# Kernel optimization log

Measured on AMD Instinct MI355X. Metric: run time of the kernel, lower is better.

The kernel has to match this reference:

```python
import jax, jax.numpy as jnp
import numpy as np

D_MODEL = 768
NUM_HEADS = 12
D_K = D_MODEL // NUM_HEADS
D_FF = 3072
EPS = 1e-5


def _layer_norm(x, gamma, beta):
    mu = jnp.mean(x, axis=-1, keepdims=True)
    var = jnp.mean(jnp.square(x - mu), axis=-1, keepdims=True)
    return (x - mu) * jax.lax.rsqrt(var + EPS) * gamma + beta


def setup_inputs() -> dict:
    key = jax.random.key(0)
    ks = jax.random.split(key, 16)
    s = 1.0 / np.sqrt(D_MODEL)
    sf = 1.0 / np.sqrt(D_FF)
    inp = {
        "x": jax.random.normal(ks[0], (2, 2048, D_MODEL), dtype=jnp.float32),
        "Wq": jax.random.uniform(ks[1], (D_MODEL, D_MODEL), jnp.float32, -s, s),
        "bq": jax.random.uniform(ks[2], (D_MODEL,), jnp.float32, -s, s),
        "Wk": jax.random.uniform(ks[3], (D_MODEL, D_MODEL), jnp.float32, -s, s),
        "bk": jax.random.uniform(ks[4], (D_MODEL,), jnp.float32, -s, s),
        "Wv": jax.random.uniform(ks[5], (D_MODEL, D_MODEL), jnp.float32, -s, s),
        "bv": jax.random.uniform(ks[6], (D_MODEL,), jnp.float32, -s, s),
        "Wo": jax.random.uniform(ks[7], (D_MODEL, D_MODEL), jnp.float32, -s, s),
        "bo": jax.random.uniform(ks[8], (D_MODEL,), jnp.float32, -s, s),
        "W1": jax.random.uniform(ks[9], (D_MODEL, D_FF), jnp.float32, -s, s),
        "b1": jax.random.uniform(ks[10], (D_FF,), jnp.float32, -s, s),
        "W2": jax.random.uniform(ks[11], (D_FF, D_MODEL), jnp.float32, -sf, sf),
        "b2": jax.random.uniform(ks[12], (D_MODEL,), jnp.float32, -sf, sf),
        "g1": jnp.ones((D_MODEL,), jnp.float32),
        "be1": jnp.zeros((D_MODEL,), jnp.float32),
        "g2": jnp.ones((D_MODEL,), jnp.float32),
        "be2": jnp.zeros((D_MODEL,), jnp.float32),
    }
    return inp


def reference(x, Wq, bq, Wk, bk, Wv, bv, Wo, bo, W1, b1, W2, b2, g1, be1, g2, be2):
    B, S, _ = x.shape

    def split(h):  # (B,S,D) -> (B,H,S,Dk)
        return h.reshape(B, S, NUM_HEADS, D_K).transpose(0, 2, 1, 3)

    q = split(x @ Wq + bq)
    k = split(x @ Wk + bk)
    v = split(x @ Wv + bv)

    # naive attention: materialize full (B,H,S,S) scores as in the original
    scores = jnp.einsum("bhsd,bhtd->bhst", q, k) / np.sqrt(D_K)
    attn = jax.nn.softmax(scores, axis=-1)
    ctx = jnp.einsum("bhst,bhtd->bhsd", attn, v)
    ctx = ctx.transpose(0, 2, 1, 3).reshape(B, S, D_MODEL)
    attn_out = ctx @ Wo + bo

    x = _layer_norm(x + attn_out, g1, be1)
    ff = jax.nn.relu(x @ W1 + b1) @ W2 + b2
    x = _layer_norm(x + ff, g2, be2)
    return x
```

## Files before the change

### kernel.cpp

```cpp
#include <hip/hip_runtime.h>
#include <cstdint>


typedef unsigned short u16;
typedef unsigned int u32;
typedef __attribute__((ext_vector_type(4))) float f32x4;
typedef __attribute__((ext_vector_type(8))) short s16x8;
typedef __attribute__((ext_vector_type(4))) u16  u16x4;
typedef __attribute__((ext_vector_type(2))) u32  u32x2;

#define AS1 __attribute__((address_space(1)))
#define AS3 __attribute__((address_space(3)))

__device__ __forceinline__ u16 f2b(float f) {
  union { float f; unsigned u; } v; v.f = f;
  unsigned r = v.u + 0x7FFFu + ((v.u >> 16) & 1u);
  return (u16)(r >> 16);
}

__device__ __forceinline__ void gl_lds16(const void* g, void* lds_uniform_base) {
  __builtin_amdgcn_global_load_lds((const AS1 void*)g, (AS3 void*)lds_uniform_base, 16, 0, 0);
}

__device__ __forceinline__ f32x4 mfma16(s16x8 a, s16x8 b, f32x4 c) {
  return __builtin_amdgcn_mfma_f32_16x16x32_bf16(a, b, c, 0, 0, 0);
}

__device__ __forceinline__ u32 cvt_pk_bf16(float lo, float hi) {
  u32 r;
  asm("v_cvt_pk_bf16_f32 %0, %1, %2" : "=v"(r) : "v"(lo), "v"(hi));
  return r;
}


__global__ __launch_bounds__(256) void transpose_conv(const float* __restrict__ W,
                                                      u16* __restrict__ Wt, int K, int N) {
  __shared__ float tile[32][33];
  int n0 = blockIdx.x * 32, k0 = blockIdx.y * 32;
  int x = threadIdx.x, y = threadIdx.y;
#pragma unroll
  for (int yy = 0; yy < 32; yy += 8)
    tile[y + yy][x] = W[(size_t)(k0 + y + yy) * N + n0 + x];
  __syncthreads();
#pragma unroll
  for (int yy = 0; yy < 32; yy += 8)
    Wt[(size_t)(n0 + y + yy) * K + k0 + x] = f2b(tile[x][y + yy]);
}

__global__ __launch_bounds__(256) void transpose_v(const u16* __restrict__ Vh,
                                                   u16* __restrict__ Vt) {
  __shared__ u16 tile[32][33];
  int bh = blockIdx.z;
  int d0 = blockIdx.x * 32, s0 = blockIdx.y * 32;
  const u16* src = Vh + (size_t)bh * 2048 * 64;
  u16* dst = Vt + (size_t)bh * 64 * 2048;
  int x = threadIdx.x, y = threadIdx.y;
#pragma unroll
  for (int yy = 0; yy < 32; yy += 8)
    tile[y + yy][x] = src[(size_t)(s0 + y + yy) * 64 + d0 + x];
  __syncthreads();
#pragma unroll
  for (int yy = 0; yy < 32; yy += 8)
    dst[(size_t)(d0 + y + yy) * 2048 + s0 + x] = tile[x][y + yy];
}

__global__ __launch_bounds__(256) void conv_bf16(const float* __restrict__ in,
                                                 u16* __restrict__ out) {
  size_t i = ((size_t)blockIdx.x * 256 + threadIdx.x) * 4;
  f32x4 v = *(const f32x4*)(in + i);
  u16x4 o;
#pragma unroll
  for (int k = 0; k < 4; ++k) o[k] = f2b(v[k]);
  *(u16x4*)(out + i) = o;
}

__global__ void concat_bias(const float* __restrict__ bq, const float* __restrict__ bk,
                            const float* __restrict__ bv, float* __restrict__ o) {
  int i = blockIdx.x * 256 + threadIdx.x;
  o[i] = (i < 768) ? bq[i] : (i < 1536) ? bk[i - 768] : bv[i - 1536];
}

template <int MODE>
__global__ __launch_bounds__(256) void gemm_bt(const u16* __restrict__ A,
                                               const u16* __restrict__ Bt,
                                               const float* __restrict__ bias,
                                               float* __restrict__ Cf, u16* __restrict__ Cb,
                                               u16* __restrict__ Qo, u16* __restrict__ Ko,
                                               u16* __restrict__ Vo, int M, int N, int K,
                                               int Klen) {
  __shared__ __align__(16) u16 lsA[128 * 64];
  __shared__ __align__(16) u16 lsB[128 * 64];
  const int tid = threadIdx.x;
  const int lane = tid & 63, wave = tid >> 6;
  const int lr = lane & 15, lh = lane >> 4;
  const int wr = wave >> 1, wc = wave & 1;
  const int m0 = blockIdx.y * 128;
  const int n0 = blockIdx.x * 128;
  const int kB = blockIdx.z * Klen;

  f32x4 acc[4][4];
#pragma unroll
  for (int i = 0; i < 4; ++i)
#pragma unroll
    for (int j = 0; j < 4; ++j) acc[i][j] = f32x4{0.f, 0.f, 0.f, 0.f};

  const size_t aBase = (size_t)m0 * K;
  const size_t bBase = (size_t)n0 * K;
  const int srow8 = tid >> 3;
  const int scolb = ((tid & 7) * 16) ^ ((srow8 & 7) << 4);
  const int xk = (lr & 7) << 4;

  for (int kt = kB; kt < kB + Klen; kt += 64) {
#pragma unroll
    for (int i = 0; i < 4; ++i) {
      int row = i * 32 + srow8;
      int ldsOff = i * 4096 + wave * 1024;
      gl_lds16(A + aBase + (size_t)row * K + kt + (scolb >> 1), (char*)lsA + ldsOff);
      gl_lds16(Bt + bBase + (size_t)row * K + kt + (scolb >> 1), (char*)lsB + ldsOff);
    }
    __syncthreads();
    const char* baA = (const char*)lsA;
    const char* baB = (const char*)lsB;
#pragma unroll
    for (int ks = 0; ks < 2; ++ks) {
      int cb = (ks * 64 + lh * 16) ^ xk;
      s16x8 a[4], b[4];
#pragma unroll
      for (int i = 0; i < 4; ++i) {
        a[i] = *(const s16x8*)(baA + (wr * 64 + i * 16 + lr) * 128 + cb);
        b[i] = *(const s16x8*)(baB + (wc * 64 + i * 16 + lr) * 128 + cb);
      }
#pragma unroll
      for (int i = 0; i < 4; ++i)
#pragma unroll
        for (int j = 0; j < 4; ++j) acc[i][j] = mfma16(a[i], b[j], acc[i][j]);
    }
    __syncthreads();
  }

  float* CfP = Cf + (size_t)blockIdx.z * M * N;
#pragma unroll
  for (int i = 0; i < 4; ++i) {
    int growb = m0 + wr * 64 + i * 16 + lh * 4;
#pragma unroll
    for (int j = 0; j < 4; ++j) {
      int col = n0 + wc * 64 + j * 16 + lr;
      float bv = (MODE != 0 || blockIdx.z == 0) ? bias[col] : 0.f;
#pragma unroll
      for (int q = 0; q < 4; ++q) {
        int grow = growb + q;
        float v = acc[i][j][q] + bv;
        if (MODE == 0) {
          CfP[(size_t)grow * N + col] = v;
        } else if (MODE == 1) {
          Cb[(size_t)grow * N + col] = f2b(fmaxf(v, 0.f));
        } else {
          int sel = col / 768;
          int c2 = col - sel * 768;
          int h = c2 >> 6, d = c2 & 63;
          int b = grow >> 11, s = grow & 2047;
          size_t idx = (((size_t)(b * 12 + h)) * 2048 + s) * 64 + d;
          float vv = (sel == 0) ? v * 0.1803368801f : v;
          u16* dst = (sel == 0) ? Qo : (sel == 1) ? Ko : Vo;
          dst[idx] = f2b(vv);
        }
      }
    }
  }
}

__global__ __launch_bounds__(512) void attn(const u16* __restrict__ Qh,
                                            const u16* __restrict__ Kh,
                                            const u16* __restrict__ Vt,
                                            float* __restrict__ Op,
                                            float* __restrict__ ml,
                                            int nbh, int ntile) {
  __shared__ __align__(16) u16 lsK[2][64 * 64];
  __shared__ __align__(16) u16 lsV[2][64 * 64];
  __shared__ __align__(16) u16 lsP[8][16 * 64];
  const int tid = threadIdx.x, lane = tid & 63, wave = tid >> 6;
  const int lr = lane & 15, lh = lane >> 4;

  int bx = blockIdx.x, bh = blockIdx.y, z = blockIdx.z;
  {
    int total = 16 * nbh * 2;
    if ((total & 7) == 0) {
      int lin = bx + 16 * (bh + nbh * z);
      int nl = (lin & 7) * (total >> 3) + (lin >> 3);
      bx = nl & 15;
      bh = (nl >> 4) % nbh;
      z = nl / (16 * nbh);
    }
  }
  const int q0 = bx * 128 + wave * 16;
  const size_t kvBase = (size_t)bh * 2048 * 64;
  const int tB = z * ntile;

  const int srow = tid >> 3;
  const int scol = (((tid & 7) * 16) ^ ((srow & 7) << 4)) >> 1;
  const u16* kSrcBase = Kh + kvBase + (size_t)srow * 64 + scol;
  const u16* vSrcBase = Vt + kvBase + (size_t)srow * 2048 + scol;

  s16x8 qf[2];
#pragma unroll
  for (int ks = 0; ks < 2; ++ks)
    qf[ks] = *(const s16x8*)(Qh + kvBase + (size_t)(q0 + lr) * 64 + ks * 32 + lh * 8);

  f32x4 oacc[4];
  float mrow = -1e30f, lsum = 0.f;
#pragma unroll
  for (int d = 0; d < 4; ++d) oacc[d] = f32x4{0.f, 0.f, 0.f, 0.f};

  gl_lds16(kSrcBase + (size_t)tB * 4096, (char*)lsK[0] + wave * 1024);
  gl_lds16(vSrcBase + tB * 64,           (char*)lsV[0] + wave * 1024);

  for (int it = 0; it < ntile; ++it) {
    const int cur = it & 1;
    __syncthreads();

    s16x8 kb[2][4];
#pragma unroll
    for (int ks = 0; ks < 2; ++ks)
#pragma unroll
      for (int j = 0; j < 4; ++j) {
        int r = j * 16 + lr;
        kb[ks][j] = *(const s16x8*)((const char*)lsK[cur] + r * 128 +
                                    ((ks * 64 + lh * 16) ^ ((r & 7) << 4)));
      }

    if (it + 1 < ntile) {
      int t = tB + it + 1;
      gl_lds16(kSrcBase + (size_t)t * 4096, (char*)lsK[cur ^ 1] + wave * 1024);
      gl_lds16(vSrcBase + t * 64,           (char*)lsV[cur ^ 1] + wave * 1024);
    }

    f32x4 st[4];
#pragma unroll
    for (int j = 0; j < 4; ++j) st[j] = f32x4{0.f, 0.f, 0.f, 0.f};
    __builtin_amdgcn_s_setprio(1);
#pragma unroll
    for (int ks = 0; ks < 2; ++ks)
#pragma unroll
      for (int j = 0; j < 4; ++j) st[j] = mfma16(kb[ks][j], qf[ks], st[j]);
    __builtin_amdgcn_s_setprio(0);

    float mx;
    {
      float a0 = fmaxf(fmaxf(st[0][0], st[0][1]), fmaxf(st[0][2], st[0][3]));
      float a1 = fmaxf(fmaxf(st[1][0], st[1][1]), fmaxf(st[1][2], st[1][3]));
      float a2 = fmaxf(fmaxf(st[2][0], st[2][1]), fmaxf(st[2][2], st[2][3]));
      float a3 = fmaxf(fmaxf(st[3][0], st[3][1]), fmaxf(st[3][2], st[3][3]));
      mx = fmaxf(fmaxf(a0, a1), fmaxf(a2, a3));
      mx = fmaxf(mx, __shfl_xor(mx, 16));
      mx = fmaxf(mx, __shfl_xor(mx, 32));
    }
    if (__any(mx > mrow + 11.f)) {
      float mn = fmaxf(mrow, mx);
      float al = exp2f(mrow - mn);
      mrow = mn;
      lsum *= al;
#pragma unroll
      for (int d = 0; d < 4; ++d)
#pragma unroll
        for (int q = 0; q < 4; ++q) oacc[d][q] *= al;
    }

    float ps = 0.f;
#pragma unroll
    for (int j = 0; j < 4; ++j) {
      float p0 = exp2f(st[j][0] - mrow);
      float p1 = exp2f(st[j][1] - mrow);
      float p2 = exp2f(st[j][2] - mrow);
      float p3 = exp2f(st[j][3] - mrow);
      ps += (p0 + p1) + (p2 + p3);
      u32x2 pk;
      pk.x = cvt_pk_bf16(p0, p1);
      pk.y = cvt_pk_bf16(p2, p3);
      *(u32x2*)((char*)lsP[wave] + lr * 128 + ((j * 32 + lh * 8) ^ ((lr & 7) << 4))) = pk;
    }
    ps += __shfl_xor(ps, 16);
    ps += __shfl_xor(ps, 32);
    lsum += ps;

    __builtin_amdgcn_s_setprio(1);
#pragma unroll
    for (int ks = 0; ks < 2; ++ks) {
      s16x8 pa = *(const s16x8*)((const char*)lsP[wave] + lr * 128 +
                                 ((ks * 64 + lh * 16) ^ ((lr & 7) << 4)));
#pragma unroll
      for (int d = 0; d < 4; ++d) {
        int r = d * 16 + lr;
        s16x8 vb = *(const s16x8*)((const char*)lsV[cur] + r * 128 +
                                   ((ks * 64 + lh * 16) ^ ((r & 7) << 4)));
        oacc[d] = mfma16(vb, pa, oacc[d]);
      }
    }
    __builtin_amdgcn_s_setprio(0);
  }

  {
    int s = q0 + lr;
    size_t r = ((size_t)z * nbh + bh) * 2048 + s;
#pragma unroll
    for (int d = 0; d < 4; ++d)
      *(f32x4*)(Op + r * 64 + d * 16 + lh * 4) = oacc[d];
    if (lh == 0) { ml[r * 2] = mrow; ml[r * 2 + 1] = lsum; }
  }
}

__global__ __launch_bounds__(256) void attn_combine(const float* __restrict__ Op,
                                                    const float* __restrict__ ml,
                                                    u16* __restrict__ ctx, int nbh) {
  size_t i = (size_t)blockIdx.x * 256 + threadIdx.x;
  int d4 = (int)(i & 15);
  size_t rs = i >> 4;
  size_t zs = (size_t)nbh * 2048;
  float m0 = ml[rs * 2],        l0 = ml[rs * 2 + 1];
  float m1 = ml[(zs + rs) * 2], l1 = ml[(zs + rs) * 2 + 1];
  float mx = fmaxf(m0, m1);
  float a0 = exp2f(m0 - mx), a1 = exp2f(m1 - mx);
  float inv = 1.f / (l0 * a0 + l1 * a1);
  a0 *= inv; a1 *= inv;
  f32x4 o0 = *(const f32x4*)(Op + rs * 64 + d4 * 4);
  f32x4 o1 = *(const f32x4*)(Op + (zs + rs) * 64 + d4 * 4);
  int bh = (int)(rs >> 11), s = (int)(rs & 2047);
  int b = bh / 12, h = bh - b * 12;
  u16x4 r;
#pragma unroll
  for (int k = 0; k < 4; ++k) r[k] = f2b(o0[k] * a0 + o1[k] * a1);
  *(u16x4*)(ctx + ((size_t)(b * 2048 + s)) * 768 + h * 64 + d4 * 4) = r;
}

template <int NP>
__global__ __launch_bounds__(256) void resid_ln(const float* __restrict__ xin,
                                                const float* __restrict__ yp,
                                                size_t pstride,
                                                const float* __restrict__ gamma,
                                                const float* __restrict__ beta,
                                                float* __restrict__ outf,
                                                u16* __restrict__ outb) {
  const int row = blockIdx.x, t = threadIdx.x;
  const size_t base = (size_t)row * 768;
  float v[3], s = 0.f, s2 = 0.f;
#pragma unroll
  for (int k = 0; k < 3; ++k) {
    int c = t + k * 256;
    float val = xin[base + c];
#pragma unroll
    for (int p = 0; p < NP; ++p) val += yp[p * pstride + base + c];
    v[k] = val; s += val; s2 += val * val;
  }
#pragma unroll
  for (int off = 32; off > 0; off >>= 1) {
    s += __shfl_down(s, off, 64);
    s2 += __shfl_down(s2, off, 64);
  }
  __shared__ float red[8];
  int lane = t & 63, wave = t >> 6;
  if (lane == 0) { red[wave] = s; red[4 + wave] = s2; }
  __syncthreads();
  s = red[0] + red[1] + red[2] + red[3];
  s2 = red[4] + red[5] + red[6] + red[7];
  const float inv = 1.f / 768.f;
  float mu = s * inv;
  float var = fmaxf(s2 * inv - mu * mu, 0.f);
  float rs = rsqrtf(var + 1e-5f);
#pragma unroll
  for (int k = 0; k < 3; ++k) {
    int c = t + k * 256;
    float o = (v[k] - mu) * rs * gamma[c] + beta[c];
    if (outf) outf[base + c] = o;
    if (outb) outb[base + c] = f2b(o);
  }
}

extern "C" void kernel_launch(void* const* d_in, const int* in_sizes, int n_in,
                              void* d_out, int out_size, void* d_ws, size_t ws_size,
                              hipStream_t stream) {
  const float* x   = (const float*)d_in[0];
  const float* Wq  = (const float*)d_in[1];
  const float* bq  = (const float*)d_in[2];
  const float* Wk  = (const float*)d_in[3];
  const float* bk  = (const float*)d_in[4];
  const float* Wv  = (const float*)d_in[5];
  const float* bv  = (const float*)d_in[6];
  const float* Wo  = (const float*)d_in[7];
  const float* bo  = (const float*)d_in[8];
  const float* W1  = (const float*)d_in[9];
  const float* b1  = (const float*)d_in[10];
  const float* W2  = (const float*)d_in[11];
  const float* b2  = (const float*)d_in[12];
  const float* g1  = (const float*)d_in[13];
  const float* be1 = (const float*)d_in[14];
  const float* g2  = (const float*)d_in[15];
  const float* be2 = (const float*)d_in[16];
  float* out = (float*)d_out;

  const int M = in_sizes[0] / 768;
  const int B = M / 2048;
  const int nbh = B * 12;

  char* ws = (char*)d_ws;
  size_t off = 0;
  auto alloc = [&](size_t bytes) -> void* {
    void* p = ws + off;
    off += (bytes + 255) & ~(size_t)255;
    return p;
  };
  u16*   Wqkv_t = (u16*)alloc((size_t)2304 * 768 * 2);
  u16*   Wo_t   = (u16*)alloc((size_t)768 * 768 * 2);
  u16*   W1_t   = (u16*)alloc((size_t)3072 * 768 * 2);
  u16*   W2_t   = (u16*)alloc((size_t)768 * 3072 * 2);
  float* bqkv   = (float*)alloc(2304 * 4);
  u16*   Xb     = (u16*)alloc((size_t)M * 768 * 2);
  u16*   Qh     = (u16*)alloc((size_t)M * 768 * 2);
  u16*   Kh     = (u16*)alloc((size_t)M * 768 * 2);
  u16*   Vh     = (u16*)alloc((size_t)M * 768 * 2);
  u16*   Vt     = (u16*)alloc((size_t)M * 768 * 2);

  size_t opElems = (size_t)2 * nbh * 2048 * 64;
  size_t mlElems = (size_t)2 * nbh * 2048 * 2;
  size_t attnBytes = (opElems + mlElems) * 4;
  size_t pstride = (size_t)M * 768;
  size_t fixedRest = pstride * 4  + pstride * 2  +
                     (size_t)M * 3072 * 2  + 4096 ;
  size_t need4 = off + ((pstride * 4 * 4 > attnBytes ? pstride * 4 * 4 : attnBytes)) + fixedRest;
  const int SPLIT2 = (ws_size >= need4) ? 4 : 2;
  size_t regionBytes = pstride * 4 * SPLIT2;
  if (regionBytes < attnBytes) regionBytes = attnBytes;
  float* region = (float*)alloc(regionBytes);
  float* Op   = region;
  float* ml   = region + opElems;
  float* ffnPart  = region;
  float* projPart = (float*)Qh;
  float* x1f  = (float*)alloc(pstride * 4);
  u16*   x1b  = (u16*)alloc(pstride * 2);
  u16*   hb   = (u16*)alloc((size_t)M * 3072 * 2);
  u16*   ctx  = Xb;

  dim3 tb(32, 8);
  transpose_conv<<<dim3(24, 24), tb, 0, stream>>>(Wq, Wqkv_t, 768, 768);
  transpose_conv<<<dim3(24, 24), tb, 0, stream>>>(Wk, Wqkv_t + (size_t)768 * 768, 768, 768);
  transpose_conv<<<dim3(24, 24), tb, 0, stream>>>(Wv, Wqkv_t + (size_t)1536 * 768, 768, 768);
  transpose_conv<<<dim3(24, 24), tb, 0, stream>>>(Wo, Wo_t, 768, 768);
  transpose_conv<<<dim3(96, 24), tb, 0, stream>>>(W1, W1_t, 768, 3072);
  transpose_conv<<<dim3(24, 96), tb, 0, stream>>>(W2, W2_t, 3072, 768);
  concat_bias<<<9, 256, 0, stream>>>(bq, bk, bv, bqkv);
  conv_bf16<<<(M * 768) / 1024, 256, 0, stream>>>(x, Xb);

  gemm_bt<2><<<dim3(2304 / 128, M / 128), 256, 0, stream>>>(
      Xb, Wqkv_t, bqkv, nullptr, nullptr, Qh, Kh, Vh, M, 2304, 768, 768);

  transpose_v<<<dim3(2, 64, nbh), tb, 0, stream>>>(Vh, Vt);

  attn<<<dim3(16, nbh, 2), 512, 0, stream>>>(Qh, Kh, Vt, Op, ml, nbh, 16);
  attn_combine<<<nbh * 128, 256, 0, stream>>>(Op, ml, ctx, nbh);

  gemm_bt<0><<<dim3(768 / 128, M / 128, 2), 256, 0, stream>>>(
      ctx, Wo_t, bo, projPart, nullptr, nullptr, nullptr, nullptr, M, 768, 768, 384);

  resid_ln<2><<<M, 256, 0, stream>>>(x, projPart, pstride, g1, be1, x1f, x1b);

  gemm_bt<1><<<dim3(3072 / 128, M / 128), 256, 0, stream>>>(
      x1b, W1_t, b1, nullptr, hb, nullptr, nullptr, nullptr, M, 3072, 768, 768);

  if (SPLIT2 == 4) {
    gemm_bt<0><<<dim3(768 / 128, M / 128, 4), 256, 0, stream>>>(
        hb, W2_t, b2, ffnPart, nullptr, nullptr, nullptr, nullptr, M, 768, 3072, 768);
    resid_ln<4><<<M, 256, 0, stream>>>(x1f, ffnPart, pstride, g2, be2, out, nullptr);
  } else {
    gemm_bt<0><<<dim3(768 / 128, M / 128, 2), 256, 0, stream>>>(
        hb, W2_t, b2, ffnPart, nullptr, nullptr, nullptr, nullptr, M, 768, 3072, 1536);
    resid_ln<2><<<M, 256, 0, stream>>>(x1f, ffnPart, pstride, g2, be2, out, nullptr);
  }
}
```

Baseline: 231.8 us.

## Fuse prep kernels, double-buffer GEMM LDS, and give attention waves two query tiles

Eight weight-transpose, bias-concat and input-conversion launches become one prep kernel, cutting launch overhead. The GEMM now double-buffers its LDS tiles, so the next K tile loads while the current one is multiplied, and one barrier per iteration is dropped. The attention kernel moves to 256 threads, with each wave handling 32 query rows instead of 16, so every K/V fragment read from LDS is reused across two MFMA tiles. The trade-off is more registers and twice the GEMM LDS footprint, which may lower occupancy.

```diff
diff --git a/kernel.cpp b/kernel.cpp
--- a/kernel.cpp
+++ b/kernel.cpp
@@ -32,19 +32,51 @@
   return r;
 }
 
-
-__global__ __launch_bounds__(256) void transpose_conv(const float* __restrict__ W,
-                                                      u16* __restrict__ Wt, int K, int N) {
-  __shared__ float tile[32][33];
-  int n0 = blockIdx.x * 32, k0 = blockIdx.y * 32;
-  int x = threadIdx.x, y = threadIdx.y;
-#pragma unroll
-  for (int yy = 0; yy < 32; yy += 8)
-    tile[y + yy][x] = W[(size_t)(k0 + y + yy) * N + n0 + x];
-  __syncthreads();
-#pragma unroll
-  for (int yy = 0; yy < 32; yy += 8)
-    Wt[(size_t)(n0 + y + yy) * K + k0 + x] = f2b(tile[x][y + yy]);
+__global__ __launch_bounds__(256) void prep(
+    const float* __restrict__ Wq, const float* __restrict__ Wk,
+    const float* __restrict__ Wv, const float* __restrict__ Wo,
+    const float* __restrict__ W1, const float* __restrict__ W2,
+    const float* __restrict__ bq, const float* __restrict__ bk,
+    const float* __restrict__ bv, const float* __restrict__ x,
+    u16* __restrict__ Wqkv_t, u16* __restrict__ Wo_t,
+    u16* __restrict__ W1_t, u16* __restrict__ W2_t,
+    float* __restrict__ bqkv, u16* __restrict__ Xb, int convBlocks) {
+  __shared__ float ts[32][33];
+  const int bid = blockIdx.x;
+  const int tx = threadIdx.x, ty = threadIdx.y;
+  if (bid < 6912) {
+    const float* W; u16* Wt; int K, N, tile;
+    if (bid < 2304) {
+      int w = bid / 576; tile = bid - w * 576; K = 768; N = 768;
+      W = (w == 0) ? Wq : (w == 1) ? Wk : (w == 2) ? Wv : Wo;
+      Wt = (w < 3) ? Wqkv_t + (size_t)w * 768 * 768 : Wo_t;
+    } else if (bid < 4608) {
+      tile = bid - 2304; K = 768; N = 3072; W = W1; Wt = W1_t;
+    } else {
+      tile = bid - 4608; K = 3072; N = 768; W = W2; Wt = W2_t;
+    }
+    int ntx = N >> 5;
+    int n0 = (tile % ntx) * 32, k0 = (tile / ntx) * 32;
+#pragma unroll
+    for (int yy = 0; yy < 32; yy += 8)
+      ts[ty + yy][tx] = W[(size_t)(k0 + ty + yy) * N + n0 + tx];
+    __syncthreads();
+#pragma unroll
+    for (int yy = 0; yy < 32; yy += 8)
+      Wt[(size_t)(n0 + ty + yy) * K + k0 + tx] = f2b(ts[tx][ty + yy]);
+  } else if (bid < 6912 + convBlocks) {
+    int t = ty * 32 + tx;
+    size_t i = ((size_t)(bid - 6912) * 256 + t) * 4;
+    f32x4 v = *(const f32x4*)(x + i);
+    u16x4 o;
+#pragma unroll
+    for (int k = 0; k < 4; ++k) o[k] = f2b(v[k]);
+    *(u16x4*)(Xb + i) = o;
+  } else {
+    int t = ty * 32 + tx;
+    int i = (bid - 6912 - convBlocks) * 256 + t;
+    if (i < 2304) bqkv[i] = (i < 768) ? bq[i] : (i < 1536) ? bk[i - 768] : bv[i - 1536];
+  }
 }
 
 __global__ __launch_bounds__(256) void transpose_v(const u16* __restrict__ Vh,
@@ -64,22 +96,6 @@
     dst[(size_t)(d0 + y + yy) * 2048 + s0 + x] = tile[x][y + yy];
 }
 
-__global__ __launch_bounds__(256) void conv_bf16(const float* __restrict__ in,
-                                                 u16* __restrict__ out) {
-  size_t i = ((size_t)blockIdx.x * 256 + threadIdx.x) * 4;
-  f32x4 v = *(const f32x4*)(in + i);
-  u16x4 o;
-#pragma unroll
-  for (int k = 0; k < 4; ++k) o[k] = f2b(v[k]);
-  *(u16x4*)(out + i) = o;
-}
-
-__global__ void concat_bias(const float* __restrict__ bq, const float* __restrict__ bk,
-                            const float* __restrict__ bv, float* __restrict__ o) {
-  int i = blockIdx.x * 256 + threadIdx.x;
-  o[i] = (i < 768) ? bq[i] : (i < 1536) ? bk[i - 768] : bv[i - 1536];
-}
-
 template <int MODE>
 __global__ __launch_bounds__(256) void gemm_bt(const u16* __restrict__ A,
                                                const u16* __restrict__ Bt,
@@ -88,8 +104,8 @@
                                                u16* __restrict__ Qo, u16* __restrict__ Ko,
                                                u16* __restrict__ Vo, int M, int N, int K,
                                                int Klen) {
-  __shared__ __align__(16) u16 lsA[128 * 64];
-  __shared__ __align__(16) u16 lsB[128 * 64];
+  __shared__ __align__(16) u16 lsA[2][128 * 64];
+  __shared__ __align__(16) u16 lsB[2][128 * 64];
   const int tid = threadIdx.x;
   const int lane = tid & 63, wave = tid >> 6;
   const int lr = lane & 15, lh = lane >> 4;
@@ -107,20 +123,27 @@
   const size_t aBase = (size_t)m0 * K;
   const size_t bBase = (size_t)n0 * K;
   const int srow8 = tid >> 3;
-  const int scolb = ((tid & 7) * 16) ^ ((srow8 & 7) << 4);
+  const int scolE = (((tid & 7) * 16) ^ ((srow8 & 7) << 4)) >> 1;
   const int xk = (lr & 7) << 4;
 
-  for (int kt = kB; kt < kB + Klen; kt += 64) {
+  auto stage = [&](int buf, int kt) {
 #pragma unroll
     for (int i = 0; i < 4; ++i) {
       int row = i * 32 + srow8;
-      int ldsOff = i * 4096 + wave * 1024;
-      gl_lds16(A + aBase + (size_t)row * K + kt + (scolb >> 1), (char*)lsA + ldsOff);
-      gl_lds16(Bt + bBase + (size_t)row * K + kt + (scolb >> 1), (char*)lsB + ldsOff);
-    }
+      int ldsOff = buf * 16384 + i * 4096 + wave * 1024;
+      gl_lds16(A + aBase + (size_t)row * K + kt + scolE, (char*)lsA + ldsOff);
+      gl_lds16(Bt + bBase + (size_t)row * K + kt + scolE, (char*)lsB + ldsOff);
+    }
+  };
+
+  const int nk = Klen >> 6;
+  stage(0, kB);
+  for (int t = 0; t < nk; ++t) {
+    const int cur = t & 1;
     __syncthreads();
-    const char* baA = (const char*)lsA;
-    const char* baB = (const char*)lsB;
+    if (t + 1 < nk) stage(cur ^ 1, kB + (t + 1) * 64);
+    const char* baA = (const char*)lsA + cur * 16384;
+    const char* baB = (const char*)lsB + cur * 16384;
 #pragma unroll
     for (int ks = 0; ks < 2; ++ks) {
       int cb = (ks * 64 + lh * 16) ^ xk;
@@ -135,7 +158,6 @@
 #pragma unroll
         for (int j = 0; j < 4; ++j) acc[i][j] = mfma16(a[i], b[j], acc[i][j]);
     }
-    __syncthreads();
   }
 
   float* CfP = Cf + (size_t)blockIdx.z * M * N;
@@ -169,15 +191,15 @@
   }
 }
 
-__global__ __launch_bounds__(512) void attn(const u16* __restrict__ Qh,
-                                            const u16* __restrict__ Kh,
-                                            const u16* __restrict__ Vt,
-                                            float* __restrict__ Op,
-                                            float* __restrict__ ml,
-                                            int nbh, int ntile) {
+__global__ __launch_bounds__(256, 3) void attn(const u16* __restrict__ Qh,
+                                               const u16* __restrict__ Kh,
+                                               const u16* __restrict__ Vt,
+                                               float* __restrict__ Op,
+                                               float* __restrict__ ml,
+                                               int nbh, int ntile) {
   __shared__ __align__(16) u16 lsK[2][64 * 64];
   __shared__ __align__(16) u16 lsV[2][64 * 64];
-  __shared__ __align__(16) u16 lsP[8][16 * 64];
+  __shared__ __align__(16) u16 lsP[4][32 * 64];
   const int tid = threadIdx.x, lane = tid & 63, wave = tid >> 6;
   const int lr = lane & 15, lh = lane >> 4;
 
@@ -192,28 +214,42 @@
       z = nl / (16 * nbh);
     }
   }
-  const int q0 = bx * 128 + wave * 16;
+  const int q0 = bx * 128 + wave * 32;
   const size_t kvBase = (size_t)bh * 2048 * 64;
   const int tB = z * ntile;
 
   const int srow = tid >> 3;
-  const int scol = (((tid & 7) * 16) ^ ((srow & 7) << 4)) >> 1;
-  const u16* kSrcBase = Kh + kvBase + (size_t)srow * 64 + scol;
-  const u16* vSrcBase = Vt + kvBase + (size_t)srow * 2048 + scol;
-
-  s16x8 qf[2];
-#pragma unroll
-  for (int ks = 0; ks < 2; ++ks)
-    qf[ks] = *(const s16x8*)(Qh + kvBase + (size_t)(q0 + lr) * 64 + ks * 32 + lh * 8);
-
-  f32x4 oacc[4];
-  float mrow = -1e30f, lsum = 0.f;
-#pragma unroll
-  for (int d = 0; d < 4; ++d) oacc[d] = f32x4{0.f, 0.f, 0.f, 0.f};
-
-  gl_lds16(kSrcBase + (size_t)tB * 4096, (char*)lsK[0] + wave * 1024);
-  gl_lds16(vSrcBase + tB * 64,           (char*)lsV[0] + wave * 1024);
-
+  const int scolE = (((tid & 7) * 16) ^ ((srow & 7) << 4)) >> 1;
+  const u16* kSrc = Kh + kvBase + (size_t)srow * 64 + scolE;
+  const u16* vSrc = Vt + kvBase + (size_t)srow * 2048 + scolE;
+
+  s16x8 qf[2][2];
+#pragma unroll
+  for (int i = 0; i < 2; ++i)
+#pragma unroll
+    for (int ks = 0; ks < 2; ++ks)
+      qf[i][ks] = *(const s16x8*)(Qh + kvBase + (size_t)(q0 + i * 16 + lr) * 64 +
+                                  ks * 32 + lh * 8);
+
+  f32x4 oacc[2][4];
+  float mrow[2], lsum[2];
+#pragma unroll
+  for (int i = 0; i < 2; ++i) {
+    mrow[i] = -1e30f; lsum[i] = 0.f;
+#pragma unroll
+    for (int d = 0; d < 4; ++d) oacc[i][d] = f32x4{0.f, 0.f, 0.f, 0.f};
+  }
+
+  auto stageKV = [&](int buf, int t) {
+#pragma unroll
+    for (int ii = 0; ii < 2; ++ii) {
+      int ldsOff = ii * 4096 + wave * 1024;
+      gl_lds16(kSrc + (size_t)(t * 64 + ii * 32) * 64, (char*)lsK[buf] + ldsOff);
+      gl_lds16(vSrc + (size_t)ii * 32 * 2048 + t * 64, (char*)lsV[buf] + ldsOff);
+    }
+  };
+
+  stageKV(0, tB);
   for (int it = 0; it < ntile; ++it) {
     const int cur = it & 1;
     __syncthreads();
@@ -228,83 +264,98 @@
                                     ((ks * 64 + lh * 16) ^ ((r & 7) << 4)));
       }
 
-    if (it + 1 < ntile) {
-      int t = tB + it + 1;
-      gl_lds16(kSrcBase + (size_t)t * 4096, (char*)lsK[cur ^ 1] + wave * 1024);
-      gl_lds16(vSrcBase + t * 64,           (char*)lsV[cur ^ 1] + wave * 1024);
-    }
-
-    f32x4 st[4];
-#pragma unroll
-    for (int j = 0; j < 4; ++j) st[j] = f32x4{0.f, 0.f, 0.f, 0.f};
+    if (it + 1 < ntile) stageKV(cur ^ 1, tB + it + 1);
+
+    f32x4 st[2][4];
+#pragma unroll
+    for (int i = 0; i < 2; ++i)
+#pragma unroll
+      for (int j = 0; j < 4; ++j) st[i][j] = f32x4{0.f, 0.f, 0.f, 0.f};
     __builtin_amdgcn_s_setprio(1);
 #pragma unroll
     for (int ks = 0; ks < 2; ++ks)
 #pragma unroll
-      for (int j = 0; j < 4; ++j) st[j] = mfma16(kb[ks][j], qf[ks], st[j]);
+      for (int j = 0; j < 4; ++j)
+#pragma unroll
+        for (int i = 0; i < 2; ++i)
+          st[i][j] = mfma16(kb[ks][j], qf[i][ks], st[i][j]);
     __builtin_amdgcn_s_setprio(0);
 
-    float mx;
-    {
-      float a0 = fmaxf(fmaxf(st[0][0], st[0][1]), fmaxf(st[0][2], st[0][3]));
-      float a1 = fmaxf(fmaxf(st[1][0], st[1][1]), fmaxf(st[1][2], st[1][3]));
-      float a2 = fmaxf(fmaxf(st[2][0], st[2][1]), fmaxf(st[2][2], st[2][3]));
-      float a3 = fmaxf(fmaxf(st[3][0], st[3][1]), fmaxf(st[3][2], st[3][3]));
-      mx = fmaxf(fmaxf(a0, a1), fmaxf(a2, a3));
-      mx = fmaxf(mx, __shfl_xor(mx, 16));
-      mx = fmaxf(mx, __shfl_xor(mx, 32));
-    }
-    if (__any(mx > mrow + 11.f)) {
-      float mn = fmaxf(mrow, mx);
-      float al = exp2f(mrow - mn);
-      mrow = mn;
-      lsum *= al;
-#pragma unroll
-      for (int d = 0; d < 4; ++d)
-#pragma unroll
-        for (int q = 0; q < 4; ++q) oacc[d][q] *= al;
-    }
-
-    float ps = 0.f;
-#pragma unroll
-    for (int j = 0; j < 4; ++j) {
-      float p0 = exp2f(st[j][0] - mrow);
-      float p1 = exp2f(st[j][1] - mrow);
-      float p2 = exp2f(st[j][2] - mrow);
-      float p3 = exp2f(st[j][3] - mrow);
-      ps += (p0 + p1) + (p2 + p3);
-      u32x2 pk;
-      pk.x = cvt_pk_bf16(p0, p1);
-      pk.y = cvt_pk_bf16(p2, p3);
-      *(u32x2*)((char*)lsP[wave] + lr * 128 + ((j * 32 + lh * 8) ^ ((lr & 7) << 4))) = pk;
-    }
-    ps += __shfl_xor(ps, 16);
-    ps += __shfl_xor(ps, 32);
-    lsum += ps;
+    float mx[2];
+    bool need = false;
+#pragma unroll
+    for (int i = 0; i < 2; ++i) {
+      float a0 = fmaxf(fmaxf(st[i][0][0], st[i][0][1]), fmaxf(st[i][0][2], st[i][0][3]));
+      float a1 = fmaxf(fmaxf(st[i][1][0], st[i][1][1]), fmaxf(st[i][1][2], st[i][1][3]));
+      float a2 = fmaxf(fmaxf(st[i][2][0], st[i][2][1]), fmaxf(st[i][2][2], st[i][2][3]));
+      float a3 = fmaxf(fmaxf(st[i][3][0], st[i][3][1]), fmaxf(st[i][3][2], st[i][3][3]));
+      float m = fmaxf(fmaxf(a0, a1), fmaxf(a2, a3));
+      m = fmaxf(m, __shfl_xor(m, 16));
+      m = fmaxf(m, __shfl_xor(m, 32));
+      mx[i] = m;
+      need = need || (m > mrow[i] + 11.f);
+    }
+    if (__any(need)) {
+#pragma unroll
+      for (int i = 0; i < 2; ++i) {
+        float mn = fmaxf(mrow[i], mx[i]);
+        float al = exp2f(mrow[i] - mn);
+        mrow[i] = mn;
+        lsum[i] *= al;
+#pragma unroll
+        for (int d = 0; d < 4; ++d)
+#pragma unroll
+          for (int q = 0; q < 4; ++q) oacc[i][d][q] *= al;
+      }
+    }
+#pragma unroll
+    for (int i = 0; i < 2; ++i) {
+      float ps = 0.f;
+#pragma unroll
+      for (int j = 0; j < 4; ++j) {
+        float p0 = exp2f(st[i][j][0] - mrow[i]);
+        float p1 = exp2f(st[i][j][1] - mrow[i]);
+        float p2 = exp2f(st[i][j][2] - mrow[i]);
+        float p3 = exp2f(st[i][j][3] - mrow[i]);
+        ps += (p0 + p1) + (p2 + p3);
+        u32x2 pk;
+        pk.x = cvt_pk_bf16(p0, p1);
+        pk.y = cvt_pk_bf16(p2, p3);
+        *(u32x2*)((char*)lsP[wave] + (i * 16 + lr) * 128 +
+                  ((j * 32 + lh * 8) ^ ((lr & 7) << 4))) = pk;
+      }
+      ps += __shfl_xor(ps, 16);
+      ps += __shfl_xor(ps, 32);
+      lsum[i] += ps;
+    }
 
     __builtin_amdgcn_s_setprio(1);
 #pragma unroll
     for (int ks = 0; ks < 2; ++ks) {
-      s16x8 pa = *(const s16x8*)((const char*)lsP[wave] + lr * 128 +
-                                 ((ks * 64 + lh * 16) ^ ((lr & 7) << 4)));
+      s16x8 pa0 = *(const s16x8*)((const char*)lsP[wave] + lr * 128 +
+                                  ((ks * 64 + lh * 16) ^ ((lr & 7) << 4)));
+      s16x8 pa1 = *(const s16x8*)((const char*)lsP[wave] + (16 + lr) * 128 +
+                                  ((ks * 64 + lh * 16) ^ ((lr & 7) << 4)));
 #pragma unroll
       for (int d = 0; d < 4; ++d) {
         int r = d * 16 + lr;
         s16x8 vb = *(const s16x8*)((const char*)lsV[cur] + r * 128 +
                                    ((ks * 64 + lh * 16) ^ ((r & 7) << 4)));
-        oacc[d] = mfma16(vb, pa, oacc[d]);
+        oacc[0][d] = mfma16(vb, pa0, oacc[0][d]);
+        oacc[1][d] = mfma16(vb, pa1, oacc[1][d]);
       }
     }
     __builtin_amdgcn_s_setprio(0);
   }
 
-  {
-    int s = q0 + lr;
+#pragma unroll
+  for (int i = 0; i < 2; ++i) {
+    int s = q0 + i * 16 + lr;
     size_t r = ((size_t)z * nbh + bh) * 2048 + s;
 #pragma unroll
     for (int d = 0; d < 4; ++d)
-      *(f32x4*)(Op + r * 64 + d * 16 + lh * 4) = oacc[d];
-    if (lh == 0) { ml[r * 2] = mrow; ml[r * 2 + 1] = lsum; }
+      *(f32x4*)(Op + r * 64 + d * 16 + lh * 4) = oacc[i][d];
+    if (lh == 0) { ml[r * 2] = mrow[i]; ml[r * 2 + 1] = lsum[i]; }
   }
 }
 
@@ -423,7 +474,7 @@
   size_t attnBytes = (opElems + mlElems) * 4;
   size_t pstride = (size_t)M * 768;
   size_t fixedRest = pstride * 4  + pstride * 2  +
-                     (size_t)M * 3072 * 2  + 4096 ;
+                     (size_t)M * 3072 * 2  + 4096;
   size_t need4 = off + ((pstride * 4 * 4 > attnBytes ? pstride * 4 * 4 : attnBytes)) + fixedRest;
   const int SPLIT2 = (ws_size >= need4) ? 4 : 2;
   size_t regionBytes = pstride * 4 * SPLIT2;
@@ -439,21 +490,17 @@
   u16*   ctx  = Xb;
 
   dim3 tb(32, 8);
-  transpose_conv<<<dim3(24, 24), tb, 0, stream>>>(Wq, Wqkv_t, 768, 768);
-  transpose_conv<<<dim3(24, 24), tb, 0, stream>>>(Wk, Wqkv_t + (size_t)768 * 768, 768, 768);
-  transpose_conv<<<dim3(24, 24), tb, 0, stream>>>(Wv, Wqkv_t + (size_t)1536 * 768, 768, 768);
-  transpose_conv<<<dim3(24, 24), tb, 0, stream>>>(Wo, Wo_t, 768, 768);
-  transpose_conv<<<dim3(96, 24), tb, 0, stream>>>(W1, W1_t, 768, 3072);
-  transpose_conv<<<dim3(24, 96), tb, 0, stream>>>(W2, W2_t, 3072, 768);
-  concat_bias<<<9, 256, 0, stream>>>(bq, bk, bv, bqkv);
-  conv_bf16<<<(M * 768) / 1024, 256, 0, stream>>>(x, Xb);
+  const int convBlocks = (M * 768) / 1024;
+  prep<<<6912 + convBlocks + 9, tb, 0, stream>>>(
+      Wq, Wk, Wv, Wo, W1, W2, bq, bk, bv, x,
+      Wqkv_t, Wo_t, W1_t, W2_t, bqkv, Xb, convBlocks);
 
   gemm_bt<2><<<dim3(2304 / 128, M / 128), 256, 0, stream>>>(
       Xb, Wqkv_t, bqkv, nullptr, nullptr, Qh, Kh, Vh, M, 2304, 768, 768);
 
   transpose_v<<<dim3(2, 64, nbh), tb, 0, stream>>>(Vh, Vt);
 
-  attn<<<dim3(16, nbh, 2), 512, 0, stream>>>(Qh, Kh, Vt, Op, ml, nbh, 16);
+  attn<<<dim3(16, nbh, 2), 256, 0, stream>>>(Qh, Kh, Vt, Op, ml, nbh, 16);
   attn_combine<<<nbh * 128, 256, 0, stream>>>(Op, ml, ctx, nbh);
 
   gemm_bt<0><<<dim3(768 / 128, M / 128, 2), 256, 0, stream>>>(
```

New measurement: 218.8 us. -5.6%, faster.

## Merge prep kernels, swizzle GEMM block order, and allow 4-way attention KV split

Applied to the files above, without the earlier changes.

Folds the six weight transpose-convert launches, the bias concat and the input bf16 conversion into one prep kernel that dispatches on block index, cutting launch count. Adds an XCD-aware block remap to all GEMM launches so neighbouring tiles land on the same die for L2 reuse. Lets attention split the key range four ways when workspace allows, with a templated combine kernel merging the partials. The deeper split adds partial-output traffic and combine work in exchange for more parallel blocks.

```diff
diff --git a/kernel.cpp b/kernel.cpp
--- a/kernel.cpp
+++ b/kernel.cpp
@@ -32,19 +32,51 @@
   return r;
 }
 
-
-__global__ __launch_bounds__(256) void transpose_conv(const float* __restrict__ W,
-                                                      u16* __restrict__ Wt, int K, int N) {
-  __shared__ float tile[32][33];
-  int n0 = blockIdx.x * 32, k0 = blockIdx.y * 32;
-  int x = threadIdx.x, y = threadIdx.y;
-#pragma unroll
-  for (int yy = 0; yy < 32; yy += 8)
-    tile[y + yy][x] = W[(size_t)(k0 + y + yy) * N + n0 + x];
-  __syncthreads();
-#pragma unroll
-  for (int yy = 0; yy < 32; yy += 8)
-    Wt[(size_t)(n0 + y + yy) * K + k0 + x] = f2b(tile[x][y + yy]);
+__global__ __launch_bounds__(256) void prep(
+    const float* __restrict__ Wq, const float* __restrict__ Wk,
+    const float* __restrict__ Wv, const float* __restrict__ Wo,
+    const float* __restrict__ W1, const float* __restrict__ W2,
+    const float* __restrict__ bq, const float* __restrict__ bk,
+    const float* __restrict__ bv, const float* __restrict__ x,
+    u16* __restrict__ Wqkv_t, u16* __restrict__ Wo_t,
+    u16* __restrict__ W1_t, u16* __restrict__ W2_t,
+    float* __restrict__ bqkv, u16* __restrict__ Xb, int convBlocks) {
+  __shared__ float ts[32][33];
+  const int bid = blockIdx.x;
+  const int tx = threadIdx.x, ty = threadIdx.y;
+  if (bid < 6912) {
+    const float* W; u16* Wt; int K, N, tile;
+    if (bid < 2304) {
+      int w = bid / 576; tile = bid - w * 576; K = 768; N = 768;
+      W = (w == 0) ? Wq : (w == 1) ? Wk : (w == 2) ? Wv : Wo;
+      Wt = (w < 3) ? Wqkv_t + (size_t)w * 768 * 768 : Wo_t;
+    } else if (bid < 4608) {
+      tile = bid - 2304; K = 768; N = 3072; W = W1; Wt = W1_t;
+    } else {
+      tile = bid - 4608; K = 3072; N = 768; W = W2; Wt = W2_t;
+    }
+    int ntx = N >> 5;
+    int n0 = (tile % ntx) * 32, k0 = (tile / ntx) * 32;
+#pragma unroll
+    for (int yy = 0; yy < 32; yy += 8)
+      ts[ty + yy][tx] = W[(size_t)(k0 + ty + yy) * N + n0 + tx];
+    __syncthreads();
+#pragma unroll
+    for (int yy = 0; yy < 32; yy += 8)
+      Wt[(size_t)(n0 + ty + yy) * K + k0 + tx] = f2b(ts[tx][ty + yy]);
+  } else if (bid < 6912 + convBlocks) {
+    int t = ty * 32 + tx;
+    size_t i = ((size_t)(bid - 6912) * 256 + t) * 4;
+    f32x4 v = *(const f32x4*)(x + i);
+    u16x4 o;
+#pragma unroll
+    for (int k = 0; k < 4; ++k) o[k] = f2b(v[k]);
+    *(u16x4*)(Xb + i) = o;
+  } else {
+    int t = ty * 32 + tx;
+    int i = (bid - 6912 - convBlocks) * 256 + t;
+    if (i < 2304) bqkv[i] = (i < 768) ? bq[i] : (i < 1536) ? bk[i - 768] : bv[i - 1536];
+  }
 }
 
 __global__ __launch_bounds__(256) void transpose_v(const u16* __restrict__ Vh,
@@ -62,22 +94,6 @@
 #pragma unroll
   for (int yy = 0; yy < 32; yy += 8)
     dst[(size_t)(d0 + y + yy) * 2048 + s0 + x] = tile[x][y + yy];
-}
-
-__global__ __launch_bounds__(256) void conv_bf16(const float* __restrict__ in,
-                                                 u16* __restrict__ out) {
-  size_t i = ((size_t)blockIdx.x * 256 + threadIdx.x) * 4;
-  f32x4 v = *(const f32x4*)(in + i);
-  u16x4 o;
-#pragma unroll
-  for (int k = 0; k < 4; ++k) o[k] = f2b(v[k]);
-  *(u16x4*)(out + i) = o;
-}
-
-__global__ void concat_bias(const float* __restrict__ bq, const float* __restrict__ bk,
-                            const float* __restrict__ bv, float* __restrict__ o) {
-  int i = blockIdx.x * 256 + threadIdx.x;
-  o[i] = (i < 768) ? bq[i] : (i < 1536) ? bk[i - 768] : bv[i - 1536];
 }
 
 template <int MODE>
@@ -94,9 +110,25 @@
   const int lane = tid & 63, wave = tid >> 6;
   const int lr = lane & 15, lh = lane >> 4;
   const int wr = wave >> 1, wc = wave & 1;
-  const int m0 = blockIdx.y * 128;
-  const int n0 = blockIdx.x * 128;
-  const int kB = blockIdx.z * Klen;
+
+  int bx, by, bz;
+  {
+    int nx = gridDim.x, ny = gridDim.y, nz = gridDim.z;
+    int total = nx * ny * nz;
+    int lin = blockIdx.x + nx * (blockIdx.y + ny * blockIdx.z);
+    if ((total & 7) == 0) {
+      int key = (lin & 7) * (total >> 3) + (lin >> 3);
+      by = key % ny;
+      int t2 = key / ny;
+      bz = t2 % nz;
+      bx = t2 / nz;
+    } else {
+      bx = blockIdx.x; by = blockIdx.y; bz = blockIdx.z;
+    }
+  }
+  const int m0 = by * 128;
+  const int n0 = bx * 128;
+  const int kB = bz * Klen;
 
   f32x4 acc[4][4];
 #pragma unroll
@@ -107,7 +139,7 @@
   const size_t aBase = (size_t)m0 * K;
   const size_t bBase = (size_t)n0 * K;
   const int srow8 = tid >> 3;
-  const int scolb = ((tid & 7) * 16) ^ ((srow8 & 7) << 4);
+  const int scolE = (((tid & 7) * 16) ^ ((srow8 & 7) << 4)) >> 1;
   const int xk = (lr & 7) << 4;
 
   for (int kt = kB; kt < kB + Klen; kt += 64) {
@@ -115,8 +147,8 @@
     for (int i = 0; i < 4; ++i) {
       int row = i * 32 + srow8;
       int ldsOff = i * 4096 + wave * 1024;
-      gl_lds16(A + aBase + (size_t)row * K + kt + (scolb >> 1), (char*)lsA + ldsOff);
-      gl_lds16(Bt + bBase + (size_t)row * K + kt + (scolb >> 1), (char*)lsB + ldsOff);
+      gl_lds16(A + aBase + (size_t)row * K + kt + scolE, (char*)lsA + ldsOff);
+      gl_lds16(Bt + bBase + (size_t)row * K + kt + scolE, (char*)lsB + ldsOff);
     }
     __syncthreads();
     const char* baA = (const char*)lsA;
@@ -138,14 +170,14 @@
     __syncthreads();
   }
 
-  float* CfP = Cf + (size_t)blockIdx.z * M * N;
+  float* CfP = Cf + (size_t)bz * M * N;
 #pragma unroll
   for (int i = 0; i < 4; ++i) {
     int growb = m0 + wr * 64 + i * 16 + lh * 4;
 #pragma unroll
     for (int j = 0; j < 4; ++j) {
       int col = n0 + wc * 64 + j * 16 + lr;
-      float bv = (MODE != 0 || blockIdx.z == 0) ? bias[col] : 0.f;
+      float bv = (MODE != 0 || bz == 0) ? bias[col] : 0.f;
 #pragma unroll
       for (int q = 0; q < 4; ++q) {
         int grow = growb + q;
@@ -183,7 +215,8 @@
 
   int bx = blockIdx.x, bh = blockIdx.y, z = blockIdx.z;
   {
-    int total = 16 * nbh * 2;
+    int nz = gridDim.z;
+    int total = 16 * nbh * nz;
     if ((total & 7) == 0) {
       int lin = bx + 16 * (bh + nbh * z);
       int nl = (lin & 7) * (total >> 3) + (lin >> 3);
@@ -308,6 +341,7 @@
   }
 }
 
+template <int NZ>
 __global__ __launch_bounds__(256) void attn_combine(const float* __restrict__ Op,
                                                     const float* __restrict__ ml,
                                                     u16* __restrict__ ctx, int nbh) {
@@ -315,19 +349,30 @@
   int d4 = (int)(i & 15);
   size_t rs = i >> 4;
   size_t zs = (size_t)nbh * 2048;
-  float m0 = ml[rs * 2],        l0 = ml[rs * 2 + 1];
-  float m1 = ml[(zs + rs) * 2], l1 = ml[(zs + rs) * 2 + 1];
-  float mx = fmaxf(m0, m1);
-  float a0 = exp2f(m0 - mx), a1 = exp2f(m1 - mx);
-  float inv = 1.f / (l0 * a0 + l1 * a1);
-  a0 *= inv; a1 *= inv;
-  f32x4 o0 = *(const f32x4*)(Op + rs * 64 + d4 * 4);
-  f32x4 o1 = *(const f32x4*)(Op + (zs + rs) * 64 + d4 * 4);
+  float m[NZ], l[NZ];
+  float mx = -1e30f;
+#pragma unroll
+  for (int p = 0; p < NZ; ++p) {
+    m[p] = ml[(p * zs + rs) * 2];
+    l[p] = ml[(p * zs + rs) * 2 + 1];
+    mx = fmaxf(mx, m[p]);
+  }
+  float wsum = 0.f, a[NZ];
+#pragma unroll
+  for (int p = 0; p < NZ; ++p) { a[p] = exp2f(m[p] - mx); wsum += l[p] * a[p]; }
+  float inv = 1.f / wsum;
+  f32x4 o = f32x4{0.f, 0.f, 0.f, 0.f};
+#pragma unroll
+  for (int p = 0; p < NZ; ++p) {
+    f32x4 op = *(const f32x4*)(Op + (p * zs + rs) * 64 + d4 * 4);
+#pragma unroll
+    for (int k = 0; k < 4; ++k) o[k] += op[k] * a[p];
+  }
   int bh = (int)(rs >> 11), s = (int)(rs & 2047);
   int b = bh / 12, h = bh - b * 12;
   u16x4 r;
 #pragma unroll
-  for (int k = 0; k < 4; ++k) r[k] = f2b(o0[k] * a0 + o1[k] * a1);
+  for (int k = 0; k < 4; ++k) r[k] = f2b(o[k] * inv);
   *(u16x4*)(ctx + ((size_t)(b * 2048 + s)) * 768 + h * 64 + d4 * 4) = r;
 }
 
@@ -418,19 +463,24 @@
   u16*   Vh     = (u16*)alloc((size_t)M * 768 * 2);
   u16*   Vt     = (u16*)alloc((size_t)M * 768 * 2);
 
-  size_t opElems = (size_t)2 * nbh * 2048 * 64;
-  size_t mlElems = (size_t)2 * nbh * 2048 * 2;
-  size_t attnBytes = (opElems + mlElems) * 4;
   size_t pstride = (size_t)M * 768;
   size_t fixedRest = pstride * 4  + pstride * 2  +
-                     (size_t)M * 3072 * 2  + 4096 ;
-  size_t need4 = off + ((pstride * 4 * 4 > attnBytes ? pstride * 4 * 4 : attnBytes)) + fixedRest;
-  const int SPLIT2 = (ws_size >= need4) ? 4 : 2;
-  size_t regionBytes = pstride * 4 * SPLIT2;
-  if (regionBytes < attnBytes) regionBytes = attnBytes;
+                     (size_t)M * 3072 * 2  + 4096;
+  auto attnBytes = [&](int nz) {
+    return (size_t)nz * nbh * 2048 * (64 + 2) * 4;
+  };
+  size_t reg4 = attnBytes(4) > pstride * 16 ? attnBytes(4) : pstride * 16;
+  int ZSPLIT, FSPLIT;
+  size_t regionBytes;
+  if (off + reg4 + fixedRest <= ws_size) {
+    ZSPLIT = 4; FSPLIT = 4; regionBytes = reg4;
+  } else {
+    ZSPLIT = 2; FSPLIT = 2;
+    regionBytes = attnBytes(2) > pstride * 8 ? attnBytes(2) : pstride * 8;
+  }
   float* region = (float*)alloc(regionBytes);
   float* Op   = region;
-  float* ml   = region + opElems;
+  float* ml   = region + (size_t)ZSPLIT * nbh * 2048 * 64;
   float* ffnPart  = region;
   float* projPart = (float*)Qh;
   float* x1f  = (float*)alloc(pstride * 4);
@@ -439,22 +489,21 @@
   u16*   ctx  = Xb;
 
   dim3 tb(32, 8);
-  transpose_conv<<<dim3(24, 24), tb, 0, stream>>>(Wq, Wqkv_t, 768, 768);
-  transpose_conv<<<dim3(24, 24), tb, 0, stream>>>(Wk, Wqkv_t + (size_t)768 * 768, 768, 768);
-  transpose_conv<<<dim3(24, 24), tb, 0, stream>>>(Wv, Wqkv_t + (size_t)1536 * 768, 768, 768);
-  transpose_conv<<<dim3(24, 24), tb, 0, stream>>>(Wo, Wo_t, 768, 768);
-  transpose_conv<<<dim3(96, 24), tb, 0, stream>>>(W1, W1_t, 768, 3072);
-  transpose_conv<<<dim3(24, 96), tb, 0, stream>>>(W2, W2_t, 3072, 768);
-  concat_bias<<<9, 256, 0, stream>>>(bq, bk, bv, bqkv);
-  conv_bf16<<<(M * 768) / 1024, 256, 0, stream>>>(x, Xb);
+  const int convBlocks = (M * 768) / 1024;
+  prep<<<6912 + convBlocks + 9, tb, 0, stream>>>(
+      Wq, Wk, Wv, Wo, W1, W2, bq, bk, bv, x,
+      Wqkv_t, Wo_t, W1_t, W2_t, bqkv, Xb, convBlocks);
 
   gemm_bt<2><<<dim3(2304 / 128, M / 128), 256, 0, stream>>>(
       Xb, Wqkv_t, bqkv, nullptr, nullptr, Qh, Kh, Vh, M, 2304, 768, 768);
 
   transpose_v<<<dim3(2, 64, nbh), tb, 0, stream>>>(Vh, Vt);
 
-  attn<<<dim3(16, nbh, 2), 512, 0, stream>>>(Qh, Kh, Vt, Op, ml, nbh, 16);
-  attn_combine<<<nbh * 128, 256, 0, stream>>>(Op, ml, ctx, nbh);
+  attn<<<dim3(16, nbh, ZSPLIT), 512, 0, stream>>>(Qh, Kh, Vt, Op, ml, nbh, 32 / ZSPLIT);
+  if (ZSPLIT == 4)
+    attn_combine<4><<<nbh * 128, 256, 0, stream>>>(Op, ml, ctx, nbh);
+  else
+    attn_combine<2><<<nbh * 128, 256, 0, stream>>>(Op, ml, ctx, nbh);
 
   gemm_bt<0><<<dim3(768 / 128, M / 128, 2), 256, 0, stream>>>(
       ctx, Wo_t, bo, projPart, nullptr, nullptr, nullptr, nullptr, M, 768, 768, 384);
@@ -464,7 +513,7 @@
   gemm_bt<1><<<dim3(3072 / 128, M / 128), 256, 0, stream>>>(
       x1b, W1_t, b1, nullptr, hb, nullptr, nullptr, nullptr, M, 3072, 768, 768);
 
-  if (SPLIT2 == 4) {
+  if (FSPLIT == 4) {
     gemm_bt<0><<<dim3(768 / 128, M / 128, 4), 256, 0, stream>>>(
         hb, W2_t, b2, ffnPart, nullptr, nullptr, nullptr, nullptr, M, 768, 3072, 768);
     resid_ln<4><<<M, 256, 0, stream>>>(x1f, ffnPart, pstride, g2, be2, out, nullptr);
```

Result: faster. 222.9 us (-3.9%).
